# Kernel optimization log

Measured on AMD Instinct MI355X. Metric: run time of the kernel, lower is better.

Reference implementation:

```python
import jax, jax.numpy as jnp
import numpy as np

WH = WW = 7          # window size
N_TOK = WH * WW      # 49 tokens per window
HEADS = 8
HEAD_DIM = 32
DIM = HEADS * HEAD_DIM  # 256
NW = 64              # windows per image (56x56 / 7x7)
BW = 64 * NW         # batch_images * windows = 4096


def _rel_pos_index(wh, ww):
    # Swin-style relative position index, flattened to (N*N,)
    coords = np.stack(np.meshgrid(np.arange(wh), np.arange(ww), indexing='ij'))  # (2, wh, ww)
    coords = coords.reshape(2, -1)                                               # (2, N)
    rel = coords[:, :, None] - coords[:, None, :]                                # (2, N, N)
    rel = rel.transpose(1, 2, 0).astype(np.int64)                                # (N, N, 2)
    rel[:, :, 0] += wh - 1
    rel[:, :, 1] += ww - 1
    rel[:, :, 0] *= 2 * ww - 1
    return jnp.asarray(rel.sum(-1).reshape(-1))                                  # (N*N,)

_REL_IDX = _rel_pos_index(WH, WW)


def setup_inputs() -> dict:
    key = jax.random.key(0)
    ks = jax.random.split(key, 5)
    x = jax.random.normal(ks[0], (BW, N_TOK, DIM), dtype=jnp.float32)
    mask = jnp.zeros((1, NW, 1, N_TOK, N_TOK), dtype=jnp.float32)
    w_qkv = jax.random.normal(ks[1], (DIM, 3 * HEADS * HEAD_DIM), dtype=jnp.float32) * 0.02
    b_qkv = jnp.zeros((3 * HEADS * HEAD_DIM,), dtype=jnp.float32)
    rel_table = jax.random.normal(ks[2], ((2 * WH - 1) * (2 * WW - 1), HEADS), dtype=jnp.float32) * 0.02
    w_out = jax.random.normal(ks[3], (HEADS * HEAD_DIM, DIM), dtype=jnp.float32) * 0.02
    b_out = jnp.zeros((DIM,), dtype=jnp.float32)
    return {"x": x, "mask": mask, "w_qkv": w_qkv, "b_qkv": b_qkv,
            "rel_table": rel_table, "w_out": w_out, "b_out": b_out}


def reference(x, mask, w_qkv, b_qkv, rel_table, w_out, b_out):
    bw, n, d = x.shape
    # QKV projection then split per original Rearrange:
    # 'b n (qkv h hd) -> qkv b h n hd'
    qkv = (x @ w_qkv + b_qkv).reshape(bw, n, 3, HEADS, HEAD_DIM)
    qkv = qkv.transpose(2, 0, 3, 1, 4)  # (3, bw, h, n, hd)
    q, k, v = qkv[0], qkv[1], qkv[2]
    # NOTE: original computes einsum('bnid,bnjd->bnij', k, q): a[i,j] = k_i . q_j
    a = jnp.einsum('bhid,bhjd->bhij', k, q) / jnp.sqrt(jnp.asarray(HEAD_DIM, x.dtype))
    # relative position bias: table gather then '(i j) h -> h i j'
    bias = rel_table[_REL_IDX].reshape(n, n, HEADS).transpose(2, 0, 1)  # (h, n, n)
    a = a + bias
    # mask add: '(b nW) h i j -> b nW h i j', + mask, back
    nw = mask.shape[1]
    a = a.reshape(bw // nw, nw, HEADS, n, n) + mask
    a = a.reshape(bw, HEADS, n, n)
    a = jax.nn.softmax(a, axis=-1)
    y = jnp.einsum('bhij,bhjd->bhid', a, v)        # (bw, h, n, hd)
    y = y.transpose(0, 2, 1, 3).reshape(bw, n, HEADS * HEAD_DIM)
    return y @ w_out + b_out
```

## Files before the change

kernel.cpp:

```cpp
#include <hip/hip_runtime.h>

typedef __attribute__((ext_vector_type(8))) short short8;
typedef __attribute__((ext_vector_type(4))) float f32x4;
typedef unsigned short u16;

#define NTOK 49
#define NBLK 4096
#define LOG2E 1.4426950408889634f

#define XF  0
#define QKP 16384
#define VTF 49152
#define POOLN 65536

#define WS_WQT 0
#define WS_WOT 393216
#define WS_BIAS 524288
#define WS_MKG 655360

__device__ __forceinline__ u16 f2bf(float f) {
  unsigned u = __float_as_uint(f);
  return (u16)((u + 0x7fffu + ((u >> 16) & 1u)) >> 16);
}
__device__ __forceinline__ unsigned packbf(float a, float b) {
  return (unsigned)f2bf(a) | ((unsigned)f2bf(b) << 16);
}

__device__ __forceinline__ short8 asm_frag(unsigned c0p0, unsigned c0p1,
                                           unsigned c1p0, unsigned c1p1,
                                           int srcA, int srcB, bool cSel) {
  unsigned a0 = (unsigned)__shfl((int)c0p0, srcA);
  unsigned b0 = (unsigned)__shfl((int)c1p0, srcA);
  unsigned a1 = (unsigned)__shfl((int)c0p1, srcA);
  unsigned b1 = (unsigned)__shfl((int)c1p1, srcA);
  unsigned a2 = (unsigned)__shfl((int)c0p0, srcB);
  unsigned b2 = (unsigned)__shfl((int)c1p0, srcB);
  unsigned a3 = (unsigned)__shfl((int)c0p1, srcB);
  unsigned b3 = (unsigned)__shfl((int)c1p1, srcB);
  union { unsigned u[4]; short8 s8; } r;
  r.u[0] = cSel ? b0 : a0;
  r.u[1] = cSel ? b1 : a1;
  r.u[2] = cSel ? b2 : a2;
  r.u[3] = cSel ? b3 : a3;
  return r.s8;
}

__global__ void prep_kernel(const float* __restrict__ w_qkv,
                            const float* __restrict__ w_out,
                            const float* __restrict__ rel,
                            const float* __restrict__ mask,
                            u16* __restrict__ wqTf,
                            u16* __restrict__ woTf,
                            float* __restrict__ biasf,
                            float* __restrict__ mkg) {
  const int stride = gridDim.x * blockDim.x;
  const int gid = blockIdx.x * blockDim.x + threadIdx.x;
  for (int e = gid; e < 48 * 8 * 64 * 8; e += stride) {
    int eL = e & 7, ln = (e >> 3) & 63, ks = (e >> 9) & 7, ctg = e >> 12;
    int k = ks * 32 + (ln >> 4) * 8 + eL;
    int c = ctg * 16 + (ln & 15);
    wqTf[e] = f2bf(w_qkv[k * 768 + c]);
  }
  for (int e = gid; e < 16 * 8 * 64 * 8; e += stride) {
    int eL = e & 7, ln = (e >> 3) & 63, ks = (e >> 9) & 7, ctg = e >> 12;
    int k = ks * 32 + (ln >> 4) * 8 + eL;
    int c = ctg * 16 + (ln & 15);
    woTf[e] = f2bf(w_out[k * 256 + c]);
  }
  for (int e = gid; e < 8 * 16 * 64 * 4; e += stride) {
    int rg = e & 3, ln = (e >> 2) & 63, t = (e >> 8) & 15, hh = e >> 12;
    int i = (t >> 2) * 16 + (ln & 15);
    int j = (t & 3) * 16 + (ln >> 4) * 4 + rg;
    float v;
    if (j >= NTOK) v = -1e30f;
    else if (i >= NTOK) v = 0.f;
    else {
      int dh = i / 7 - j / 7 + 6;
      int dw = i % 7 - j % 7 + 6;
      v = rel[(dh * 13 + dw) * 8 + hh];
    }
    biasf[e] = v * LOG2E;
  }
  for (int e = gid; e < 64 * 16 * 64 * 4; e += stride) {
    int rg = e & 3, ln = (e >> 2) & 63, t = (e >> 8) & 15, wdw = e >> 12;
    int i = (t >> 2) * 16 + (ln & 15);
    int j = (t & 3) * 16 + (ln >> 4) * 4 + rg;
    mkg[e] = (i < NTOK && j < NTOK) ? mask[wdw * (NTOK * NTOK) + i * NTOK + j] * LOG2E : 0.f;
  }
}

__global__ void __launch_bounds__(1024, 4) winattn_mfma(
    const float* __restrict__ x,
    const float* __restrict__ b_qkv,
    const float* __restrict__ b_out,
    const u16* __restrict__ wqTf,
    const u16* __restrict__ woTf,
    const float* __restrict__ biasf,
    const float* __restrict__ mkg,
    float* __restrict__ out)
{
  __shared__ u16 pool[POOLN];
  const int b = blockIdx.x, tid = threadIdx.x;
  const int lane = tid & 63, lo = lane & 15, hi = lane >> 4;
  const int w = tid >> 6;
  const int h = w & 7;
  const int it0 = (w >> 3) * 2;
  const f32x4 zf = {0.f, 0.f, 0.f, 0.f};

  {
    const float4* xg = (const float4*)(x + (size_t)b * (NTOK * 256));
    for (int e = tid; e < 49 * 64; e += 1024) {
      float4 v = xg[e];
      int r = e >> 6, ks = (e >> 3) & 7, sub = (e >> 1) & 3, eb = (e & 1) * 4;
      int unit = ((r >> 4) * 8 + ks) * 64 + sub * 16 + ((r & 15) ^ ((2 * sub + ks) & 15));
      *(uint2*)&pool[XF + unit * 8 + eb] = make_uint2(packbf(v.x, v.y), packbf(v.z, v.w));
    }
    if (tid < 15 * 64) {
      int e = tid;
      int r = 49 + (e >> 6), c = e & 63;
      int ks = c >> 3, sub = (c >> 1) & 3, eb = (c & 1) * 4;
      int unit = ((r >> 4) * 8 + ks) * 64 + sub * 16 + ((r & 15) ^ ((2 * sub + ks) & 15));
      *(uint2*)&pool[XF + unit * 8 + eb] = make_uint2(0u, 0u);
    }
  }
  __syncthreads();

  {
    const int ctq0 = 2 * w, ctq1 = 2 * w + 1, ctv = 32 + w;
    f32x4 acc[3][4];
    #pragma unroll
    for (int ct = 0; ct < 3; ++ct)
      #pragma unroll
      for (int rt = 0; rt < 4; ++rt) acc[ct][rt] = zf;
    const int lo2 = 2 * hi;
    #pragma unroll
    for (int ks = 0; ks < 8; ++ks) {
      const int swz = (lo ^ ((lo2 + ks) & 15));
      short8 bx[4];
      #pragma unroll
      for (int rt = 0; rt < 4; ++rt)
        bx[rt] = *(const short8*)&pool[XF + (((rt * 8 + ks) * 64) + hi * 16 + swz) * 8];
      short8 af0 = *(const short8*)&wqTf[((size_t)(ctq0 * 8 + ks) * 64 + lane) * 8];
      short8 af1 = *(const short8*)&wqTf[((size_t)(ctq1 * 8 + ks) * 64 + lane) * 8];
      short8 afv = *(const short8*)&wqTf[((size_t)(ctv * 8 + ks) * 64 + lane) * 8];
      #pragma unroll
      for (int rt = 0; rt < 4; ++rt) {
        acc[0][rt] = __builtin_amdgcn_mfma_f32_16x16x32_bf16(af0, bx[rt], acc[0][rt], 0, 0, 0);
        acc[1][rt] = __builtin_amdgcn_mfma_f32_16x16x32_bf16(af1, bx[rt], acc[1][rt], 0, 0, 0);
        acc[2][rt] = __builtin_amdgcn_mfma_f32_16x16x32_bf16(bx[rt], afv, acc[2][rt], 0, 0, 0);
      }
    }
    const int qkbase = QKP + (w & 7) * 4096 + ((w >= 8) ? 2048 : 0);
    #pragma unroll
    for (int ct = 0; ct < 2; ++ct) {
      const int ctg = 2 * w + ct;
      f32x4 bias = *(const f32x4*)(b_qkv + ctg * 16 + hi * 4);
      #pragma unroll
      for (int rt = 0; rt < 4; ++rt) {
        f32x4 v = acc[ct][rt] + bias;
        int hi2 = ct * 2 + (hi >> 1);
        int eb = (hi & 1) * 4;
        *(uint2*)&pool[qkbase + (rt * 64 + hi2 * 16 + lo) * 8 + eb] =
            make_uint2(packbf(v[0], v[1]), packbf(v[2], v[3]));
      }
    }
    {
      const int vhead = w >> 1, dblk = w & 1;
      const float bv = b_qkv[ctv * 16 + lo];
      #pragma unroll
      for (int rt = 0; rt < 4; ++rt) {
        f32x4 v = acc[2][rt];
        float v0 = v[0] + bv, v1 = v[1] + bv, v2 = v[2] + bv, v3 = v[3] + bv;
        int f = dblk * 2 + (rt >> 1);
        int hiR = (rt & 1) * 2 + (hi >> 1);
        int eb = (hi & 1) * 4;
        *(uint2*)&pool[VTF + (f * 8 + vhead) * 512 + (hiR * 16 + lo) * 8 + eb] =
            make_uint2(packbf(v0, v1), packbf(v2, v3));
      }
    }
  }
  __syncthreads();

  float rs0 = 0.f, rs1 = 0.f;
  unsigned pkp[4][2][2];
  {
    const float SC = 0.17677669529663687f * LOG2E;
    short8 ka0 = *(const short8*)&pool[QKP + h * 4096 + 2048 + ((it0 + 0) * 64 + lane) * 8];
    short8 ka1 = *(const short8*)&pool[QKP + h * 4096 + 2048 + ((it0 + 1) * 64 + lane) * 8];
    const float* bh = biasf + h * 4096;
    const float* mh = mkg + (size_t)(b & 63) * 4096;
    #pragma unroll
    for (int jt = 0; jt < 4; ++jt) {
      short8 qa = *(const short8*)&pool[QKP + h * 4096 + (jt * 64 + lane) * 8];
      f32x4 s0 = __builtin_amdgcn_mfma_f32_16x16x32_bf16(qa, ka0, zf, 0, 0, 0);
      f32x4 s1 = __builtin_amdgcn_mfma_f32_16x16x32_bf16(qa, ka1, zf, 0, 0, 0);
      {
        const int t = (it0 + 0) * 4 + jt;
        f32x4 bm = *(const f32x4*)&bh[(t * 64 + lane) * 4];
        f32x4 mm = *(const f32x4*)&mh[(t * 64 + lane) * 4];
        float p0 = exp2f(fmaf(s0[0], SC, bm[0] + mm[0]));
        float p1 = exp2f(fmaf(s0[1], SC, bm[1] + mm[1]));
        float p2 = exp2f(fmaf(s0[2], SC, bm[2] + mm[2]));
        float p3 = exp2f(fmaf(s0[3], SC, bm[3] + mm[3]));
        rs0 += (p0 + p1) + (p2 + p3);
        pkp[jt][0][0] = packbf(p0, p1);
        pkp[jt][0][1] = packbf(p2, p3);
      }
      {
        const int t = (it0 + 1) * 4 + jt;
        f32x4 bm = *(const f32x4*)&bh[(t * 64 + lane) * 4];
        f32x4 mm = *(const f32x4*)&mh[(t * 64 + lane) * 4];
        float p0 = exp2f(fmaf(s1[0], SC, bm[0] + mm[0]));
        float p1 = exp2f(fmaf(s1[1], SC, bm[1] + mm[1]));
        float p2 = exp2f(fmaf(s1[2], SC, bm[2] + mm[2]));
        float p3 = exp2f(fmaf(s1[3], SC, bm[3] + mm[3]));
        rs1 += (p0 + p1) + (p2 + p3);
        pkp[jt][1][0] = packbf(p0, p1);
        pkp[jt][1][1] = packbf(p2, p3);
      }
    }
  }
  float inv0, inv1;
  {
    float r2 = rs0 + __shfl_xor(rs0, 16);
    inv0 = 1.f / (r2 + __shfl_xor(r2, 32));
    float r3 = rs1 + __shfl_xor(rs1, 16);
    inv1 = 1.f / (r3 + __shfl_xor(r3, 32));
  }

  {
    const int srcA = lo + 32 * (hi & 1);
    const int srcB = srcA + 16;
    const bool cSel = (hi & 2) != 0;
    short8 va[2][2];
    #pragma unroll
    for (int dblk = 0; dblk < 2; ++dblk)
      #pragma unroll
      for (int k2 = 0; k2 < 2; ++k2)
        va[dblk][k2] = *(const short8*)&pool[VTF + ((dblk * 2 + k2) * 8 + h) * 512 + lane * 8];
    f32x4 ya[2][2];
    ya[0][0] = zf; ya[0][1] = zf; ya[1][0] = zf; ya[1][1] = zf;
    #pragma unroll
    for (int itL = 0; itL < 2; ++itL)
      #pragma unroll
      for (int k2 = 0; k2 < 2; ++k2) {
        short8 pb = asm_frag(pkp[2 * k2][itL][0], pkp[2 * k2][itL][1],
                             pkp[2 * k2 + 1][itL][0], pkp[2 * k2 + 1][itL][1], srcA, srcB, cSel);
        ya[0][itL] = __builtin_amdgcn_mfma_f32_16x16x32_bf16(va[0][k2], pb, ya[0][itL], 0, 0, 0);
        ya[1][itL] = __builtin_amdgcn_mfma_f32_16x16x32_bf16(va[1][k2], pb, ya[1][itL], 0, 0, 0);
      }
    #pragma unroll
    for (int itL = 0; itL < 2; ++itL) {
      const float iv = itL ? inv1 : inv0;
      #pragma unroll
      for (int dblk = 0; dblk < 2; ++dblk) {
        f32x4 yy = ya[dblk][itL];
        int hi2 = dblk * 2 + (hi >> 1);
        int eb = (hi & 1) * 4;
        *(uint2*)&pool[XF + (((it0 + itL) * 8 + h) * 64 + hi2 * 16 + lo) * 8 + eb] =
            make_uint2(packbf(yy[0] * iv, yy[1] * iv), packbf(yy[2] * iv, yy[3] * iv));
      }
    }
  }
  __syncthreads();

  {
    f32x4 pacc[4];
    pacc[0] = zf; pacc[1] = zf; pacc[2] = zf; pacc[3] = zf;
    #pragma unroll
    for (int ks = 0; ks < 8; ++ks) {
      short8 wf = *(const short8*)&woTf[((size_t)(w * 8 + ks) * 64 + lane) * 8];
      #pragma unroll
      for (int rt = 0; rt < 4; ++rt) {
        short8 yb = *(const short8*)&pool[XF + ((rt * 8 + ks) * 64 + lane) * 8];
        pacc[rt] = __builtin_amdgcn_mfma_f32_16x16x32_bf16(wf, yb, pacc[rt], 0, 0, 0);
      }
    }
    float* og = out + (size_t)b * (NTOK * 256);
    const int cb = w * 16 + hi * 4;
    f32x4 bb = *(const f32x4*)(b_out + cb);
    #pragma unroll
    for (int rt = 0; rt < 4; ++rt) {
      const int r = rt * 16 + lo;
      if (r < NTOK) {
        f32x4 vv = pacc[rt] + bb;
        *(f32x4*)(og + (size_t)r * 256 + cb) = vv;
      }
    }
  }
}

extern "C" void kernel_launch(void* const* d_in, const int* in_sizes, int n_in,
                              void* d_out, int out_size, void* d_ws, size_t ws_size,
                              hipStream_t stream) {
  const float *x = nullptr, *mask = nullptr, *w_qkv = nullptr, *b_qkv = nullptr,
              *rel_t = nullptr, *w_out = nullptr, *b_out = nullptr;
  for (int i = 0; i < n_in; ++i) {
    const float* p = (const float*)d_in[i];
    switch (in_sizes[i]) {
      case 4096 * 49 * 256: x = p; break;
      case 64 * 49 * 49:    mask = p; break;
      case 256 * 768:       w_qkv = p; break;
      case 768:             b_qkv = p; break;
      case 169 * 8:         rel_t = p; break;
      case 256 * 256:       w_out = p; break;
      case 256:             b_out = p; break;
    }
  }
  char* wsb = (char*)d_ws;
  u16* wqTf    = (u16*)(wsb + WS_WQT);
  u16* woTf    = (u16*)(wsb + WS_WOT);
  float* biasf = (float*)(wsb + WS_BIAS);
  float* mkg   = (float*)(wsb + WS_MKG);

  hipLaunchKernelGGL(prep_kernel, dim3(1024), dim3(256), 0, stream,
                     w_qkv, w_out, rel_t, mask, wqTf, woTf, biasf, mkg);
  hipLaunchKernelGGL(winattn_mfma, dim3(NBLK), dim3(1024), 0, stream,
                     x, b_qkv, b_out, wqTf, woTf, biasf, mkg, (float*)d_out);
}
```

Before: 318.9 us.

## Stage mask tile in LDS, use hardware bf16 pack, drop X swizzle

Measured after the change: 301.7 us. 1.06x faster.

```diff
diff --git a/kernel.cpp b/kernel.cpp
--- a/kernel.cpp
+++ b/kernel.cpp
@@ -11,7 +11,8 @@
 #define XF  0
 #define QKP 16384
 #define VTF 49152
-#define POOLN 65536
+#define MKF 65536
+#define POOLN 73728
 
 #define WS_WQT 0
 #define WS_WOT 393216
@@ -23,7 +24,9 @@
   return (u16)((u + 0x7fffu + ((u >> 16) & 1u)) >> 16);
 }
 __device__ __forceinline__ unsigned packbf(float a, float b) {
-  return (unsigned)f2bf(a) | ((unsigned)f2bf(b) << 16);
+  unsigned r;
+  asm("v_cvt_pk_bf16_f32 %0, %1, %2" : "=v"(r) : "v"(a), "v"(b));
+  return r;
 }
 
 __device__ __forceinline__ short8 asm_frag(unsigned c0p0, unsigned c0p1,
@@ -106,21 +109,25 @@
   const int h = w & 7;
   const int it0 = (w >> 3) * 2;
   const f32x4 zf = {0.f, 0.f, 0.f, 0.f};
+  float* mkf = (float*)(pool + MKF);
 
   {
     const float4* xg = (const float4*)(x + (size_t)b * (NTOK * 256));
     for (int e = tid; e < 49 * 64; e += 1024) {
       float4 v = xg[e];
-      int r = e >> 6, ks = (e >> 3) & 7, sub = (e >> 1) & 3, eb = (e & 1) * 4;
-      int unit = ((r >> 4) * 8 + ks) * 64 + sub * 16 + ((r & 15) ^ ((2 * sub + ks) & 15));
-      *(uint2*)&pool[XF + unit * 8 + eb] = make_uint2(packbf(v.x, v.y), packbf(v.z, v.w));
+      int r = e >> 6, c4 = (e & 63) << 2;
+      int addr = (((r >> 4) * 8 + (c4 >> 5)) * 64 + ((c4 >> 3) & 3) * 16 + (r & 15)) * 8 + (c4 & 7);
+      *(uint2*)&pool[XF + addr] = make_uint2(packbf(v.x, v.y), packbf(v.z, v.w));
     }
     if (tid < 15 * 64) {
       int e = tid;
-      int r = 49 + (e >> 6), c = e & 63;
-      int ks = c >> 3, sub = (c >> 1) & 3, eb = (c & 1) * 4;
-      int unit = ((r >> 4) * 8 + ks) * 64 + sub * 16 + ((r & 15) ^ ((2 * sub + ks) & 15));
-      *(uint2*)&pool[XF + unit * 8 + eb] = make_uint2(0u, 0u);
+      int r = 49 + (e >> 6), c4 = (e & 63) << 2;
+      int addr = (((r >> 4) * 8 + (c4 >> 5)) * 64 + ((c4 >> 3) & 3) * 16 + (r & 15)) * 8 + (c4 & 7);
+      *(uint2*)&pool[XF + addr] = make_uint2(0u, 0u);
+    }
+    const float4* mg = (const float4*)(mkg + (size_t)(b & 63) * 4096);
+    for (int e = tid; e < 1024; e += 1024) {
+      *(float4*)&mkf[e * 4] = mg[e];
     }
   }
   __syncthreads();
@@ -132,14 +139,12 @@
     for (int ct = 0; ct < 3; ++ct)
       #pragma unroll
       for (int rt = 0; rt < 4; ++rt) acc[ct][rt] = zf;
-    const int lo2 = 2 * hi;
     #pragma unroll
     for (int ks = 0; ks < 8; ++ks) {
-      const int swz = (lo ^ ((lo2 + ks) & 15));
       short8 bx[4];
       #pragma unroll
       for (int rt = 0; rt < 4; ++rt)
-        bx[rt] = *(const short8*)&pool[XF + (((rt * 8 + ks) * 64) + hi * 16 + swz) * 8];
+        bx[rt] = *(const short8*)&pool[XF + ((rt * 8 + ks) * 64 + lane) * 8];
       short8 af0 = *(const short8*)&wqTf[((size_t)(ctq0 * 8 + ks) * 64 + lane) * 8];
       short8 af1 = *(const short8*)&wqTf[((size_t)(ctq1 * 8 + ks) * 64 + lane) * 8];
       short8 afv = *(const short8*)&wqTf[((size_t)(ctv * 8 + ks) * 64 + lane) * 8];
@@ -188,7 +193,6 @@
     short8 ka0 = *(const short8*)&pool[QKP + h * 4096 + 2048 + ((it0 + 0) * 64 + lane) * 8];
     short8 ka1 = *(const short8*)&pool[QKP + h * 4096 + 2048 + ((it0 + 1) * 64 + lane) * 8];
     const float* bh = biasf + h * 4096;
-    const float* mh = mkg + (size_t)(b & 63) * 4096;
     #pragma unroll
     for (int jt = 0; jt < 4; ++jt) {
       short8 qa = *(const short8*)&pool[QKP + h * 4096 + (jt * 64 + lane) * 8];
@@ -197,7 +201,7 @@
       {
         const int t = (it0 + 0) * 4 + jt;
         f32x4 bm = *(const f32x4*)&bh[(t * 64 + lane) * 4];
-        f32x4 mm = *(const f32x4*)&mh[(t * 64 + lane) * 4];
+        f32x4 mm = *(const f32x4*)&mkf[(t * 64 + lane) * 4];
         float p0 = exp2f(fmaf(s0[0], SC, bm[0] + mm[0]));
         float p1 = exp2f(fmaf(s0[1], SC, bm[1] + mm[1]));
         float p2 = exp2f(fmaf(s0[2], SC, bm[2] + mm[2]));
@@ -209,7 +213,7 @@
       {
         const int t = (it0 + 1) * 4 + jt;
         f32x4 bm = *(const f32x4*)&bh[(t * 64 + lane) * 4];
-        f32x4 mm = *(const f32x4*)&mh[(t * 64 + lane) * 4];
+        f32x4 mm = *(const f32x4*)&mkf[(t * 64 + lane) * 4];
         float p0 = exp2f(fmaf(s1[0], SC, bm[0] + mm[0]));
         float p1 = exp2f(fmaf(s1[1], SC, bm[1] + mm[1]));
         float p2 = exp2f(fmaf(s1[2], SC, bm[2] + mm[2]));
```
